# Kernel optimization log

Measured on AMD Instinct MI355X. Metric: run time of the kernel, lower is better.

Reference implementation:

```python
import jax, jax.numpy as jnp
import numpy as np

V, E, H, L, B = 32000, 512, 512, 64, 32
H2 = 2 * H  # decoder hidden size
SOS = 127


def lstm_cell(x, h, c, Wih, Whh, b):
    gates = x @ Wih.T + h @ Whh.T + b
    i, f, g, o = jnp.split(gates, 4, axis=-1)
    i = jax.nn.sigmoid(i); f = jax.nn.sigmoid(f); o = jax.nn.sigmoid(o)
    g = jnp.tanh(g)
    c2 = f * c + i * g
    return o * jnp.tanh(c2), c2


def setup_inputs() -> dict:
    key = jax.random.key(0)
    ks = jax.random.split(key, 20)
    s = 0.02
    inp = {
        "x": jax.random.randint(ks[0], (B, L), 0, V),
        "enc_embed": s * jax.random.normal(ks[1], (V, E), jnp.float32),
        "ef_Wih": s * jax.random.normal(ks[2], (4 * H, E), jnp.float32),
        "ef_Whh": s * jax.random.normal(ks[3], (4 * H, H), jnp.float32),
        "ef_b": jnp.zeros((4 * H,), jnp.float32),
        "eb_Wih": s * jax.random.normal(ks[4], (4 * H, E), jnp.float32),
        "eb_Whh": s * jax.random.normal(ks[5], (4 * H, H), jnp.float32),
        "eb_b": jnp.zeros((4 * H,), jnp.float32),
        "dec_embed": s * jax.random.normal(ks[6], (V, H2), jnp.float32),
        "attn_W": s * jax.random.normal(ks[7], (L, 2 * H2), jnp.float32),
        "attn_b": jnp.zeros((L,), jnp.float32),
        "comb_W": s * jax.random.normal(ks[8], (H2, 2 * H2), jnp.float32),
        "comb_b": jnp.zeros((H2,), jnp.float32),
        "d_Wih": s * jax.random.normal(ks[9], (4 * H2, H2), jnp.float32),
        "d_Whh": s * jax.random.normal(ks[10], (4 * H2, H2), jnp.float32),
        "d_b": jnp.zeros((4 * H2,), jnp.float32),
        "out_W": s * jax.random.normal(ks[11], (V, H2), jnp.float32),
        "out_b": jnp.zeros((V,), jnp.float32),
    }
    return inp


def reference(x, enc_embed, ef_Wih, ef_Whh, ef_b, eb_Wih, eb_Whh, eb_b,
              dec_embed, attn_W, attn_b, comb_W, comb_b,
              d_Wih, d_Whh, d_b, out_W, out_b):
    b, seq = x.shape
    emb = enc_embed[x]  # (B, L, E)

    # Encoder: per-timestep bidirectional LSTM cells (each length-1 call),
    # state carried across the unrolled timestep loop.
    def enc_step(carry, xt):
        hf, cf, hb, cb = carry
        hf, cf = lstm_cell(xt, hf, cf, ef_Wih, ef_Whh, ef_b)
        hb, cb = lstm_cell(xt, hb, cb, eb_Wih, eb_Whh, eb_b)
        return (hf, cf, hb, cb), jnp.concatenate([hf, hb], axis=-1)

    z = jnp.zeros((b, ef_Whh.shape[1]), emb.dtype)
    _, enc_outs = jax.lax.scan(enc_step, (z, z, z, z), emb.transpose(1, 0, 2))
    enc_outs = enc_outs.transpose(1, 0, 2)  # (B, L, 2H)

    # Decoder: Bahdanau-style attention + LSTM cell, greedy argmax feedback.
    h2 = d_Whh.shape[1]

    def dec_step(carry, _):
        h, c, tok = carry
        e = dec_embed[tok]  # (B, 2H)
        aw = jax.nn.softmax(jnp.concatenate([e, h], -1) @ attn_W.T + attn_b, axis=-1)  # (B, L)
        ctx = jnp.einsum('bl,bld->bd', aw, enc_outs)  # (B, 2H)
        comb = jax.nn.relu(jnp.concatenate([e, ctx], -1) @ comb_W.T + comb_b)
        h, c = lstm_cell(comb, h, c, d_Wih, d_Whh, d_b)
        logits = jax.nn.log_softmax(h @ out_W.T + out_b, axis=-1)  # (B, V)
        tok = jnp.argmax(logits, axis=-1)
        return (h, c, tok), logits

    h0 = jnp.zeros((b, h2), emb.dtype)
    tok0 = jnp.full((b,), SOS, dtype=x.dtype)
    _, logits = jax.lax.scan(dec_step, (h0, h0, tok0), None, length=seq)
    return logits.transpose(1, 0, 2)  # (B, T, V)
```

## Files before the change

### kernel.cpp

```cpp
#include <hip/hip_runtime.h>
#include <hip/hip_bf16.h>
#include <string.h>

typedef __bf16 bf16;
typedef __attribute__((ext_vector_type(8))) __bf16 bf16x8;
typedef __attribute__((ext_vector_type(2))) __bf16 bf16x2;
typedef __attribute__((ext_vector_type(4))) float  f32x4;
typedef unsigned long long u64;
typedef unsigned char u8;

#define DEV __device__ __forceinline__

constexpr int V = 32000, E = 512, H = 512, L = 64, NB = 32, H2 = 1024, T = 64, SOS = 127;
constexpr int GE = 4 * H;
constexpr int NBLK = 256;

constexpr size_t OFF_GIN    = 0;
constexpr size_t SZ_GIN     = (size_t)2*T*NB*GE*4;
constexpr size_t OFF_ENCOUT = OFF_GIN + SZ_GIN;
constexpr size_t SZ_ENCOUT  = (size_t)NB*L*H2*2;
constexpr size_t OFF_ENCH   = OFF_ENCOUT + SZ_ENCOUT;
constexpr size_t SZ_ENCH    = (size_t)2*2*NB*H*2;
constexpr size_t OFF_DECH   = OFF_ENCH + SZ_ENCH;
constexpr size_t SZ_DECH    = (size_t)2*NB*H2*2;
constexpr size_t OFF_CAT2   = OFF_DECH + SZ_DECH;
constexpr size_t SZ_CAT2    = (size_t)NB*2*H2*2;
constexpr size_t OFF_COMB   = OFF_CAT2 + SZ_CAT2;
constexpr size_t SZ_COMB    = (size_t)NB*H2*2;
constexpr size_t OFF_HH     = OFF_COMB + SZ_COMB;
constexpr size_t SZ_HH      = (size_t)NB*4*H2*4;
constexpr size_t OFF_PMAX   = OFF_HH + SZ_HH;
constexpr size_t SZ_P       = (size_t)2*NBLK*NB*4;
constexpr size_t OFF_PSUM   = OFF_PMAX + SZ_P;
constexpr size_t OFF_PIDX   = OFF_PSUM + SZ_P;
constexpr size_t OFF_LOGZ   = OFF_PIDX + SZ_P;
constexpr size_t SZ_LOGZ    = (size_t)T*NB*4;
constexpr size_t OFF_WEFIH  = OFF_LOGZ + SZ_LOGZ;
constexpr size_t SZ_WENC    = (size_t)GE*E*2;
constexpr size_t OFF_WEFHH  = OFF_WEFIH + SZ_WENC;
constexpr size_t OFF_WEBIH  = OFF_WEFHH + SZ_WENC;
constexpr size_t OFF_WEBHH  = OFF_WEBIH + SZ_WENC;
constexpr size_t OFF_WCOMB  = OFF_WEBHH + SZ_WENC;
constexpr size_t SZ_WCOMB   = (size_t)H2*2*H2*2;
constexpr size_t OFF_WDIH   = OFF_WCOMB + SZ_WCOMB;
constexpr size_t SZ_WDEC    = (size_t)4*H2*H2*2;
constexpr size_t OFF_WDHH   = OFF_WDIH + SZ_WDEC;
constexpr size_t OFF_WOUT   = OFF_WDHH + SZ_WDEC;
constexpr size_t OFF_WOUT8  = OFF_WOUT;
constexpr size_t SZ_WOUT8   = (size_t)V*1024;
constexpr size_t OFF_WDHH8  = OFF_WOUT8 + SZ_WOUT8;
constexpr size_t SZ_WOUT    = (size_t)V*H2*2;
constexpr size_t OFF_WATTN  = OFF_WOUT + SZ_WOUT;
constexpr size_t SZ_WATTN   = (size_t)L*2*H2*2;
constexpr size_t OFF_EMB2   = OFF_WATTN + SZ_WATTN;
constexpr size_t SZ_EMB2    = (size_t)T*NB*E*2;
constexpr size_t OFF_BAR    = OFF_EMB2 + SZ_EMB2;
constexpr int TAG_PT = 0, TAG_C2 = 8192, TAG_CB = 9216, TAG_H = 11264, TAG_E = 13312;
constexpr int BAR_INTS = 15360;
constexpr size_t OFF_H8 = OFF_BAR + 131072;

constexpr int SM_HL   = 114688;
constexpr int SM_CATF = 114688;
constexpr int SM_REDM = 122880;
constexpr int SM_REDS = 124928;
constexpr int SM_REDI = 126976;
constexpr int SM_SCR  = 129024;
constexpr int SM_BYTES = 147456;

DEV f32x4 mfma16(bf16x8 a, bf16x8 b, f32x4 c) {
  return __builtin_amdgcn_mfma_f32_16x16x32_bf16(a, b, c, 0, 0, 0);
}
DEV f32x4 mfma8(long a, long b, f32x4 c) {
  return __builtin_amdgcn_mfma_f32_16x16x32_fp8_fp8(a, b, c, 0, 0, 0);
}
DEV float sigm(float x) { return 1.f / (1.f + __expf(-x)); }
DEV bf16x8 ld8(const bf16* p) { return *(const bf16x8*)p; }

union U16 { u64 u[2]; bf16x8 v8; f32x4 f4; };
union U4  { unsigned int u; bf16x2 v2; float f; };

DEV bf16x8 ld8_dev(const bf16* p) {
  U16 r;
  r.u[0] = __hip_atomic_load((const u64*)p,       __ATOMIC_RELAXED, __HIP_MEMORY_SCOPE_AGENT);
  r.u[1] = __hip_atomic_load((const u64*)(p + 4), __ATOMIC_RELAXED, __HIP_MEMORY_SCOPE_AGENT);
  return r.v8;
}
DEV void st8_dev(bf16* p, bf16x8 v) {
  U16 r; r.v8 = v;
  __hip_atomic_store((u64*)p,       r.u[0], __ATOMIC_RELAXED, __HIP_MEMORY_SCOPE_AGENT);
  __hip_atomic_store((u64*)(p + 4), r.u[1], __ATOMIC_RELAXED, __HIP_MEMORY_SCOPE_AGENT);
}
DEV void st16f_dev(float* p, f32x4 v) {
  U16 r; r.f4 = v;
  __hip_atomic_store((u64*)p,       r.u[0], __ATOMIC_RELAXED, __HIP_MEMORY_SCOPE_AGENT);
  __hip_atomic_store((u64*)(p + 2), r.u[1], __ATOMIC_RELAXED, __HIP_MEMORY_SCOPE_AGENT);
}
DEV float ldf_dev(const float* p) {
  return __hip_atomic_load(p, __ATOMIC_RELAXED, __HIP_MEMORY_SCOPE_AGENT);
}
DEV void stf_dev(float* p, float v) {
  __hip_atomic_store(p, v, __ATOMIC_RELAXED, __HIP_MEMORY_SCOPE_AGENT);
}
DEV int ldi_dev(const int* p) {
  return __hip_atomic_load(p, __ATOMIC_RELAXED, __HIP_MEMORY_SCOPE_AGENT);
}
DEV void sti_dev(int* p, int v) {
  __hip_atomic_store(p, v, __ATOMIC_RELAXED, __HIP_MEMORY_SCOPE_AGENT);
}
DEV void stb_dev(bf16* p, float x) {
  bf16 h = (bf16)x; unsigned short s; memcpy(&s, &h, 2);
  __hip_atomic_store((unsigned short*)p, s, __ATOMIC_RELAXED, __HIP_MEMORY_SCOPE_AGENT);
}
DEV void st2b_dev(bf16* p, bf16x2 v) {
  U4 r; r.v2 = v;
  __hip_atomic_store((unsigned int*)p, r.u, __ATOMIC_RELAXED, __HIP_MEMORY_SCOPE_AGENT);
}
DEV void stb8_dev(u8* p, u8 v) {
  __hip_atomic_store(p, v, __ATOMIC_RELAXED, __HIP_MEMORY_SCOPE_AGENT);
}
DEV u64 ldu64_dev(const u8* p) {
  return __hip_atomic_load((const u64*)p, __ATOMIC_RELAXED, __HIP_MEMORY_SCOPE_AGENT);
}

DEV void tpub(int* tags, int slot, int ep) {
  __syncthreads();
  if (threadIdx.x == 0)
    sti_dev(tags + slot*32, ep);
}
DEV void twait(int* tags, int n, int ep) {
  if ((int)threadIdx.x < n)
    while (ldi_dev(tags + threadIdx.x*32) < ep)
      __builtin_amdgcn_s_sleep(1);
  asm volatile("" ::: "memory");
  __syncthreads();
}

struct ConvJobs { const float* src[7]; bf16* dst[7]; long n8[7]; };

__global__ __launch_bounds__(256) void k_convert_all(ConvJobs J) {
  long i0 = (long)blockIdx.x * 256 + threadIdx.x;
  long stride = (long)gridDim.x * 256;
  for (int j = 0; j < 7; ++j) {
    const float* __restrict__ src = J.src[j];
    bf16* __restrict__ dst = J.dst[j];
    long n8 = J.n8[j];
    for (long g = i0; g < n8; g += stride) {
      long o = g * 8;
      float4 a = *(const float4*)(src + o);
      float4 b = *(const float4*)(src + o + 4);
      bf16x8 v;
      v[0]=(bf16)a.x; v[1]=(bf16)a.y; v[2]=(bf16)a.z; v[3]=(bf16)a.w;
      v[4]=(bf16)b.x; v[5]=(bf16)b.y; v[6]=(bf16)b.z; v[7]=(bf16)b.w;
      *(bf16x8*)(dst + o) = v;
    }
  }
}

__global__ __launch_bounds__(256) void k_conv_fp8(const float* __restrict__ wsrc,
                                                  const float* __restrict__ hsrc,
                                                  u8* __restrict__ wdst,
                                                  u8* __restrict__ hdst) {
  const long G1 = (long)V*64, G2 = (long)4096*64;
  for (long id = (long)blockIdx.x*256 + threadIdx.x; id < G1 + G2;
       id += (long)gridDim.x*256) {
    const float* s; u8* d; long n, g;
    if (id < G1) { n = id >> 6; g = id & 63; s = wsrc + n*1024 + g*16;
                   d = wdst + n*1024 + ((g ^ (n & 7)) << 4); }
    else { long j = id - G1; n = j >> 6; g = j & 63; s = hsrc + n*1024 + g*16;
           d = hdst + n*1024 + ((g ^ (n & 7)) << 4); }
    unsigned int wv[4];
#pragma unroll
    for (int q = 0; q < 4; ++q) {
      float4 f = *(const float4*)(s + q*4);
      int lo = __builtin_amdgcn_cvt_pk_fp8_f32(f.x*8.f, f.y*8.f, 0, false);
      int hi = __builtin_amdgcn_cvt_pk_fp8_f32(f.z*8.f, f.w*8.f, 0, false);
      wv[q] = (lo & 0xFFFF) | (hi << 16);
    }
    *(uint4*)d = make_uint4(wv[0], wv[1], wv[2], wv[3]);
  }
}

__global__ __launch_bounds__(256) void k_gather_emb(const int* __restrict__ x,
                                                    const float* __restrict__ embed,
                                                    bf16* __restrict__ emb2) {
  int gid = blockIdx.x * 256 + threadIdx.x;
  int m = gid >> 6, k8 = (gid & 63) * 8;
  int b = m & 31, t = m >> 5;
  int tok = x[b * L + t];
  const float* src = embed + (long)tok * E + k8;
  float4 a = *(const float4*)src;
  float4 c = *(const float4*)(src + 4);
  bf16x8 v;
  v[0]=(bf16)a.x; v[1]=(bf16)a.y; v[2]=(bf16)a.z; v[3]=(bf16)a.w;
  v[4]=(bf16)c.x; v[5]=(bf16)c.y; v[6]=(bf16)c.z; v[7]=(bf16)c.w;
  *(bf16x8*)(emb2 + (long)m * E + k8) = v;
}

__global__ __launch_bounds__(256) void k_init(bf16* ench, bf16* dech, float* hh,
                                              int* bar) {
  int i = blockIdx.x * 256 + threadIdx.x;
  hh[i] = 0.f;
  if (i < 2*NB*H)  ench[i] = (bf16)0.f;
  if (i < NB*H2)   dech[i] = (bf16)0.f;
  if (i < BAR_INTS) bar[i] = 0;
}

__global__ __launch_bounds__(256) void k_enc_ingemm(
    const bf16* __restrict__ emb2,
    const bf16* __restrict__ fWih, const float* __restrict__ fB,
    const bf16* __restrict__ bWih, const float* __restrict__ bB,
    float* __restrict__ gin)
{
  int wid  = blockIdx.x * 4 + (threadIdx.x >> 6);
  int lane = threadIdx.x & 63;
  int dir  = wid >> 11;
  int w2   = wid & 2047;
  int m0   = (w2 >> 5) * 32;
  int n0   = (w2 & 31) * 64;
  const bf16*  Wih  = dir ? bWih : fWih;
  const float* Bias = dir ? bB : fB;
  int col = lane & 15, kq = lane >> 4, r4 = kq * 4;

  const bf16* arow[4];
#pragma unroll
  for (int nt = 0; nt < 4; ++nt) arow[nt] = Wih + (long)(n0 + nt*16 + col)*E + kq*8;
  const bf16* brow[2];
#pragma unroll
  for (int mt = 0; mt < 2; ++mt) brow[mt] = emb2 + (long)(m0 + mt*16 + col)*E + kq*8;

  f32x4 acc[2][4] = {};
  for (int kk = 0; kk < E/32; ++kk) {
    bf16x8 a[4], bv[2];
#pragma unroll
    for (int nt = 0; nt < 4; ++nt) a[nt] = ld8(arow[nt] + kk*32);
#pragma unroll
    for (int mt = 0; mt < 2; ++mt) bv[mt] = ld8(brow[mt] + kk*32);
#pragma unroll
    for (int mt = 0; mt < 2; ++mt)
#pragma unroll
      for (int nt = 0; nt < 4; ++nt)
        acc[mt][nt] = mfma16(a[nt], bv[mt], acc[mt][nt]);
  }
#pragma unroll
  for (int mt = 0; mt < 2; ++mt) {
    int m = m0 + mt*16 + col;
    int b = m & 31, t = m >> 5;
    float* gp = gin + ((long)(dir*T + t)*NB + b)*GE;
#pragma unroll
    for (int nt = 0; nt < 4; ++nt) {
      int nb = n0 + nt*16 + r4;
      f32x4 v = acc[mt][nt];
      float4 o;
      o.x = v[0] + Bias[nb+0];
      o.y = v[1] + Bias[nb+1];
      o.z = v[2] + Bias[nb+2];
      o.w = v[3] + Bias[nb+3];
      *(float4*)(gp + nb) = o;
    }
  }
}

struct EncArgs {
  const bf16* fWhh; const bf16* bWhh; const float* gin;
  bf16* ench; bf16* encout; int* etag;
};

__global__ __launch_bounds__(256, 1) void k_encoder(EncArgs A) {
  __shared__ float lds[4][16][32];
  int tid = threadIdx.x, w = tid >> 6, lane = tid & 63;
  int dir = blockIdx.x >> 5, j0 = (blockIdx.x & 31) * 16;
  int col = lane & 15, kq = lane >> 4, r4 = kq*4;
  const bf16* Whh = dir ? A.bWhh : A.fWhh;
  const bf16* arow = Whh + (long)(w*H + j0 + col)*H + kq*8;
  int* myTags = A.etag + dir*32*32;
  float creg0 = 0.f, creg1 = 0.f;

  for (int t = 0; t < T; ++t) {
    if (t > 0) twait(myTags, 32, t);
    const bf16* hbase = A.ench + (t&1)*(2*NB*H) + dir*(NB*H);
    bf16*       hout  = A.ench + ((t&1)^1)*(2*NB*H) + dir*(NB*H);
    const bf16* b0 = hbase + col*H + kq*8;
    const bf16* b1 = hbase + (16+col)*H + kq*8;
    f32x4 a0 = {}, a1 = {};
    for (int kk = 0; kk < H/32; ++kk) {
      bf16x8 a = ld8(arow + kk*32);
      a0 = mfma16(a, ld8_dev(b0 + kk*32), a0);
      a1 = mfma16(a, ld8_dev(b1 + kk*32), a1);
    }
#pragma unroll
    for (int r = 0; r < 4; ++r) { lds[w][r4+r][col] = a0[r]; lds[w][r4+r][16+col] = a1[r]; }
    __syncthreads();
    const float* gp = A.gin + (long)(dir*T + t)*NB*GE;
    {
      int jj = tid >> 5, b = tid & 31, j = j0 + jj;
      const float* g4 = gp + (long)b*GE;
      float i_ = sigm(lds[0][jj][b] + g4[0*H + j]);
      float f_ = sigm(lds[1][jj][b] + g4[1*H + j]);
      float g_ = tanhf(lds[2][jj][b] + g4[2*H + j]);
      float o_ = sigm(lds[3][jj][b] + g4[3*H + j]);
      float c2 = f_*creg0 + i_*g_; creg0 = c2;
      float hv = o_*tanhf(c2);
      stb_dev(hout + b*H + j, hv);
      A.encout[((long)b*L + t)*H2 + dir*H + j] = (bf16)hv;
    }
    {
      int idx = tid + 256, jj = idx >> 5, b = idx & 31, j = j0 + jj;
      const float* g4 = gp + (long)b*GE;
      float i_ = sigm(lds[0][jj][b] + g4[0*H + j]);
      float f_ = sigm(lds[1][jj][b] + g4[1*H + j]);
      float g_ = tanhf(lds[2][jj][b] + g4[2*H + j]);
      float o_ = sigm(lds[3][jj][b] + g4[3*H + j]);
      float c2 = f_*creg1 + i_*g_; creg1 = c2;
      float hv = o_*tanhf(c2);
      stb_dev(hout + b*H + j, hv);
      A.encout[((long)b*L + t)*H2 + dir*H + j] = (bf16)hv;
    }
    tpub(myTags, blockIdx.x & 31, t + 1);
  }
}

struct DecArgs {
  const float* dec_embed; const bf16* wattn; const float* attn_b;
  const bf16* encout;
  const bf16* wcomb; const float* comb_b;
  const bf16* wdih; const float* db;
  const u8* wout8; const u8* wdhh8; const float* outb;
  bf16* dech; u8* hout8; float* hh; bf16* cat2; bf16* comb;
  float* pmax; float* psum; int* pidx; float* logz; float* out;
  int* tags;
};

__global__ __launch_bounds__(512, 1) void k_decoder(DecArgs A) {
  __shared__ __attribute__((aligned(16))) char smem[SM_BYTES];
  __shared__ float aw[64];
  __shared__ int   stok;
  float* catF = (float*)(smem + SM_CATF);
  float* redm = (float*)(smem + SM_REDM);
  float* reds = (float*)(smem + SM_REDS);
  int*   redi = (int*)  (smem + SM_REDI);
  float* scr  = (float*)(smem + SM_SCR);

  int* PT  = A.tags + TAG_PT;
  int* C2T = A.tags + TAG_C2;
  int* CBT = A.tags + TAG_CB;
  int* HT  = A.tags + TAG_H;

  int tid = threadIdx.x, bid = blockIdx.x;
  int w = tid >> 6, lane = tid & 63;
  int col = lane & 15, kq = lane >> 4, r4 = kq*4;
  float creg = 0.f;

  int ntot = (bid < 48) ? 8 : 9;
  int tstart = (bid < 48) ? bid*8 : 384 + 9*(bid - 48);
  const int nlds = 7;

  for (int i = 0; i < nlds; ++i) {
    int tn = tstart + i;
    const u8* src = (tn < 2000) ? A.wout8 + (long)tn*16384
                                : A.wdhh8 + (long)(tn - 2000)*16384;
#pragma unroll
    for (int rr = 0; rr < 2; ++rr) {
      int flat = rr*8192 + w*1024 + lane*16;
      __builtin_amdgcn_global_load_lds(
          (const __attribute__((address_space(1))) void*)(src + flat),
          (__attribute__((address_space(3))) void*)(smem + i*16384 + rr*8192 + w*1024),
          16, 0, 0);
    }
  }
  asm volatile("s_waitcnt vmcnt(0)" ::: "memory");
  __syncthreads();

  for (int t = 0; t < T; ++t) {
    const bf16* hin  = A.dech + (t&1)*(NB*H2);
    bf16*       hout = A.dech + ((t&1)^1)*(NB*H2);
    float* pmaxP = A.pmax + ((t&1)^1)*NBLK*32;
    float* psumP = A.psum + ((t&1)^1)*NBLK*32;
    int*   pidxP = A.pidx + ((t&1)^1)*NBLK*32;

    if (bid < NB) {
      int b = bid;
      if (t > 0) {
        twait(PT, NBLK, t);
        float m = -1e30f, s = 0.f; int id = 0;
        if (tid < 256) {
          m  = ldf_dev(pmaxP + tid*32 + b);
          s  = ldf_dev(psumP + tid*32 + b);
          id = ldi_dev(pidxP + tid*32 + b);
#pragma unroll
          for (int off = 1; off < 64; off <<= 1) {
            float om = __shfl_xor(m, off);
            float os = __shfl_xor(s, off);
            int   oi = __shfl_xor(id, off);
            s += os;
            if (om > m || (om == m && oi < id)) { m = om; id = oi; }
          }
          if (lane == 0) { redm[w] = m; reds[w] = s; redi[w] = id; }
        }
        __syncthreads();
        if (tid == 0) {
          float mm = redm[0]; int ii2 = redi[0];
          float ss = reds[0] + reds[1] + reds[2] + reds[3];
#pragma unroll
          for (int q = 1; q < 4; ++q) {
            if (redm[q] > mm || (redm[q] == mm && redi[q] < ii2)) { mm = redm[q]; ii2 = redi[q]; }
          }
          A.logz[(t-1)*32 + b] = logf(ss);
          stok = ii2;
        }
      } else if (tid == 0) stok = SOS;
      __syncthreads();
      int tok = stok;

      const float* erow = A.dec_embed + (long)tok*H2;
      bf16* c2row = A.cat2 + (long)b*(2*H2);
      if (tid < 128) {
        int o = tid*8;
        float4 a = *(const float4*)(erow + o);
        float4 c = *(const float4*)(erow + o + 4);
        catF[o+0]=a.x; catF[o+1]=a.y; catF[o+2]=a.z; catF[o+3]=a.w;
        catF[o+4]=c.x; catF[o+5]=c.y; catF[o+6]=c.z; catF[o+7]=c.w;
        bf16x8 v;
        v[0]=(bf16)a.x; v[1]=(bf16)a.y; v[2]=(bf16)a.z; v[3]=(bf16)a.w;
        v[4]=(bf16)c.x; v[5]=(bf16)c.y; v[6]=(bf16)c.z; v[7]=(bf16)c.w;
        st8_dev(c2row + o, v);
      } else if (tid < 256) {
        int o = (tid - 128)*8;
        bf16x8 hv = ld8_dev(hin + (long)b*H2 + o);
#pragma unroll
        for (int e = 0; e < 8; ++e) catF[H2 + o + e] = (float)hv[e];
      }
      __syncthreads();

      {
        int l = tid >> 3, q = tid & 7;
        const bf16*  wrow = A.wattn + (long)l*(2*H2) + q*256;
        const float* crow = catF + q*256;
        float sacc = 0.f;
        for (int k = 0; k < 256; k += 8) {
          bf16x8 wv = ld8(wrow + k);
#pragma unroll
          for (int e = 0; e < 8; ++e) sacc += (float)wv[e] * crow[k+e];
        }
        sacc += __shfl_xor(sacc, 1);
        sacc += __shfl_xor(sacc, 2);
        sacc += __shfl_xor(sacc, 4);
        if (q == 0) aw[l] = sacc + A.attn_b[l];
      }
      __syncthreads();

      if (tid < 64) {
        float v = aw[tid];
        float m = v;
#pragma unroll
        for (int off = 1; off < 64; off <<= 1) m = fmaxf(m, __shfl_xor(m, off));
        float p = __expf(v - m);
        float s = p;
#pragma unroll
        for (int off = 1; off < 64; off <<= 1) s += __shfl_xor(s, off);
        aw[tid] = p / s;
      }
      __syncthreads();

      {
        int grp = tid >> 7, jt = tid & 127;
        int j8 = jt * 8;
        const bf16* eo = A.encout + (long)b*L*H2 + j8;
        float acc[8] = {};
        for (int l = grp*16; l < grp*16 + 16; ++l) {
          float a = aw[l];
          bf16x8 v = ld8(eo + (long)l*H2);
#pragma unroll
          for (int e = 0; e < 8; ++e) acc[e] += a*(float)v[e];
        }
#pragma unroll
        for (int e = 0; e < 8; ++e) scr[grp*1024 + j8 + e] = acc[e];
      }
      __syncthreads();
      {
        int j2 = tid * 2;
        bf16x2 o;
#pragma unroll
        for (int e = 0; e < 2; ++e) {
          int j = j2 + e;
          o[e] = (bf16)(scr[j] + scr[1024+j] + scr[2048+j] + scr[3072+j]);
        }
        st2b_dev(c2row + H2 + j2, o);
      }
      tpub(C2T, bid, t + 1);
    }

    if (bid < 64) {
      twait(C2T, 32, t + 1);
      int n0 = bid * 16;
      const bf16* arow = A.wcomb + (long)(n0 + col)*(2*H2) + w*256 + kq*8;
      const bf16* b0 = A.cat2 + (long)col*(2*H2) + w*256 + kq*8;
      const bf16* b1 = A.cat2 + (long)(16+col)*(2*H2) + w*256 + kq*8;
      f32x4 a0 = {}, a1 = {};
      for (int kk = 0; kk < 8; ++kk) {
        bf16x8 a = ld8(arow + kk*32);
        a0 = mfma16(a, ld8_dev(b0 + kk*32), a0);
        a1 = mfma16(a, ld8_dev(b1 + kk*32), a1);
      }
#pragma unroll
      for (int r = 0; r < 4; ++r) {
        scr[(w*2+0)*256 + (r4+r)*16 + col] = a0[r];
        scr[(w*2+1)*256 + (r4+r)*16 + col] = a1[r];
      }
      __syncthreads();
      {
        int r = tid >> 5, b = tid & 31;
        int bt = b >> 4, cb = b & 15;
        float v = 0.f;
#pragma unroll
        for (int g = 0; g < 8; ++g) v += scr[(g*2+bt)*256 + r*16 + cb];
        v += A.comb_b[n0 + r];
        stb_dev(A.comb + (long)b*H2 + n0 + r, fmaxf(v, 0.f));
      }
      tpub(CBT, bid, t + 1);
    }

    if (bid < 64) {
      twait(CBT, 64, t + 1);
      int j0 = bid * 16;
      int g = w >> 1, half = w & 1;
      const bf16* arow = A.wdih + (long)(g*H2 + j0 + col)*H2 + half*512 + kq*8;
      const bf16* b0 = A.comb + (long)col*H2 + half*512 + kq*8;
      const bf16* b1 = A.comb + (long)(16+col)*H2 + half*512 + kq*8;
      f32x4 a0 = {}, a1 = {};
      for (int kk = 0; kk < 16; ++kk) {
        bf16x8 a = ld8(arow + kk*32);
        a0 = mfma16(a, ld8_dev(b0 + kk*32), a0);
        a1 = mfma16(a, ld8_dev(b1 + kk*32), a1);
      }
#pragma unroll
      for (int r = 0; r < 4; ++r) {
        scr[(w*2+0)*256 + (r4+r)*16 + col] = a0[r];
        scr[(w*2+1)*256 + (r4+r)*16 + col] = a1[r];
      }
      __syncthreads();
      {
        int jj = tid >> 5, b = tid & 31, j = j0 + jj;
        int bt = b >> 4, cb = b & 15;
#define GV(gg) (scr[((2*(gg)+0)*2+bt)*256 + jj*16 + cb] + scr[((2*(gg)+1)*2+bt)*256 + jj*16 + cb] \
                + A.db[(gg)*H2 + j] + ldf_dev(A.hh + (long)b*(4*H2) + (gg)*H2 + j))
        float i_ = sigm(GV(0));
        float f_ = sigm(GV(1));
        float g_ = tanhf(GV(2));
        float o_ = sigm(GV(3));
#undef GV
        float c2 = f_*creg + i_*g_; creg = c2;
        float hv = o_*tanhf(c2);
        stb_dev(hout + b*H2 + j, hv);
        int q8 = __builtin_amdgcn_cvt_pk_fp8_f32(hv*16.f, hv*16.f, 0, false);
        stb8_dev(A.hout8 + b*1024 + j, (u8)(q8 & 0xFF));
      }
      tpub(HT, bid, t + 1);
    }

    {
      twait(HT, 64, t + 1);
      float* pmaxW = A.pmax + (t&1)*NBLK*32;
      float* psumW = A.psum + (t&1)*NBLK*32;
      int*   pidxW = A.pidx + (t&1)*NBLK*32;

#pragma unroll
      for (int k2 = 0; k2 < 4; ++k2) {
        int id = k2*512 + tid;
        int r = id >> 6, g = id & 63;
        const u8* sp = A.hout8 + r*1024 + g*16;
        u64 lo = ldu64_dev(sp);
        u64 hi = ldu64_dev(sp + 8);
        char* dp = smem + SM_HL + r*1024 + ((g ^ (r & 7)) << 4);
        *(u64*)dp = lo; *(u64*)(dp + 8) = hi;
      }
      __syncthreads();

      float pm[2] = {-1e30f, -1e30f};
      float ps[2] = {0.f, 0.f};
      int  pid[2] = {0, 0};

      for (int ii = 0; ii < 2; ++ii) {
        if (ii == 1 && (w != 0 || ntot < 9)) break;
        int ti = (ii == 0) ? w : 8;
        int tn = tstart + ti;
        f32x4 acc0 = {}, acc1 = {};
        if (ti < nlds) {
          const char* Ab = smem + ti*16384 + col*1024;
          const char* Hb = smem + SM_HL + col*1024;
#pragma unroll 8
          for (int ks = 0; ks < 32; ++ks) {
            int off = (((ks*2 + (kq>>1)) ^ (col & 7)) << 4) + (kq & 1)*8;
            long a  = *(const long*)(Ab + off);
            long b0 = *(const long*)(Hb + off);
            long b1 = *(const long*)(Hb + 16*1024 + off);
            acc0 = mfma8(a, b0, acc0);
            acc1 = mfma8(a, b1, acc1);
          }
        } else {
          const u8* Ab = ((tn < 2000) ? A.wout8 + (long)tn*16384
                                      : A.wdhh8 + (long)(tn - 2000)*16384) + col*1024;
          const char* Hb = smem + SM_HL + col*1024;
#pragma unroll 8
          for (int ks = 0; ks < 32; ++ks) {
            int off = (((ks*2 + (kq>>1)) ^ (col & 7)) << 4) + (kq & 1)*8;
            long a  = (long)ldu64_dev(Ab + off);
            long b0 = *(const long*)(Hb + off);
            long b1 = *(const long*)(Hb + 16*1024 + off);
            acc0 = mfma8(a, b0, acc0);
            acc1 = mfma8(a, b1, acc1);
          }
        }
        if (tn < 2000) {
          int nb = tn*16 + kq*4;
#pragma unroll
          for (int bt = 0; bt < 2; ++bt) {
            int b = col + bt*16;
            f32x4 v = bt ? acc1 : acc0;
            f32x4 o;
#pragma unroll
            for (int r = 0; r < 4; ++r) {
              float xv = v[r]*0.0078125f + A.outb[nb + r];
              o[r] = xv;
              ps[bt] += __expf(xv);
              if (xv > pm[bt]) { pm[bt] = xv; pid[bt] = nb + r; }
            }
            __builtin_nontemporal_store(o, (f32x4*)(A.out + ((long)b*T + t)*V + nb));
          }
        } else {
          int nb = (tn - 2000)*16 + kq*4;
#pragma unroll
          for (int bt = 0; bt < 2; ++bt) {
            int b = col + bt*16;
            f32x4 v = bt ? acc1 : acc0;
#pragma unroll
            for (int r = 0; r < 4; ++r) v[r] *= 0.0078125f;
            st16f_dev(A.hh + (long)b*(4*H2) + nb, v);
          }
        }
      }
#pragma unroll
      for (int off = 16; off <= 32; off <<= 1) {
#pragma unroll
        for (int bt = 0; bt < 2; ++bt) {
          float om = __shfl_xor(pm[bt], off);
          float os = __shfl_xor(ps[bt], off);
          int   oi = __shfl_xor(pid[bt], off);
          ps[bt] += os;
          if (om > pm[bt] || (om == pm[bt] && oi < pid[bt])) { pm[bt] = om; pid[bt] = oi; }
        }
      }
      __syncthreads();
      float* dm = (float*)(smem + SM_HL);
      float* ds = dm + 256;
      int*   di = (int*)(ds + 256);
      if (lane < 16) {
#pragma unroll
        for (int bt = 0; bt < 2; ++bt) {
          int b = bt*16 + lane;
          dm[w*32 + b] = pm[bt];
          ds[w*32 + b] = ps[bt];
          di[w*32 + b] = pid[bt];
        }
      }
      __syncthreads();
      if (tid < 32) {
        int b = tid;
        float m = -1e30f, s = 0.f; int id = 0;
#pragma unroll
        for (int r = 0; r < 8; ++r) {
          float om = dm[r*32 + b]; int oi = di[r*32 + b];
          s += ds[r*32 + b];
          if (om > m || (om == m && oi < id)) { m = om; id = oi; }
        }
        stf_dev(pmaxW + bid*32 + b, m);
        stf_dev(psumW + bid*32 + b, s);
        sti_dev(pidxW + bid*32 + b, id);
      }
      tpub(PT, bid, t + 1);
    }
  }

  if (bid < NB) {
    twait(PT, NBLK, T);
    int b = bid;
    const float* psumP = A.psum + ((T-1)&1)*NBLK*32;
    float s = 0.f;
    if (tid < 256) {
      s = ldf_dev(psumP + tid*32 + b);
#pragma unroll
      for (int off = 1; off < 64; off <<= 1) s += __shfl_xor(s, off);
      if (lane == 0) reds[w] = s;
    }
    __syncthreads();
    if (tid == 0) A.logz[(T-1)*32 + b] = logf(reds[0] + reds[1] + reds[2] + reds[3]);
  }
}

__global__ __launch_bounds__(256) void k_fixup(float* __restrict__ out,
                                               const float* __restrict__ logz)
{
  long i = (long)blockIdx.x * 256 + threadIdx.x;
  long stride = (long)gridDim.x * 256;
  long total = (long)NB * T * V / 4;
  for (long g = i; g < total; g += stride) {
    long flat = g * 4;
    long bt = flat / V;
    int tt = (int)(bt & 63), b = (int)(bt >> 6);
    float lz = logz[tt*32 + b];
    f32x4 v = *(const f32x4*)(out + flat);
    v[0] -= lz; v[1] -= lz; v[2] -= lz; v[3] -= lz;
    __builtin_nontemporal_store(v, (f32x4*)(out + flat));
  }
}

extern "C" void kernel_launch(void* const* d_in, const int* in_sizes, int n_in,
                              void* d_out, int out_size, void* d_ws, size_t ws_size,
                              hipStream_t stream)
{
  const int*   x         = (const int*)  d_in[0];
  const float* enc_embed = (const float*)d_in[1];
  const float* ef_Wih    = (const float*)d_in[2];
  const float* ef_Whh    = (const float*)d_in[3];
  const float* ef_b      = (const float*)d_in[4];
  const float* eb_Wih    = (const float*)d_in[5];
  const float* eb_Whh    = (const float*)d_in[6];
  const float* eb_b      = (const float*)d_in[7];
  const float* dec_embed = (const float*)d_in[8];
  const float* attn_W    = (const float*)d_in[9];
  const float* attn_b    = (const float*)d_in[10];
  const float* comb_W    = (const float*)d_in[11];
  const float* comb_b    = (const float*)d_in[12];
  const float* d_Wih     = (const float*)d_in[13];
  const float* d_Whh     = (const float*)d_in[14];
  const float* d_b       = (const float*)d_in[15];
  const float* out_W     = (const float*)d_in[16];
  const float* out_b     = (const float*)d_in[17];
  float* out = (float*)d_out;
  char* ws = (char*)d_ws;

  float* gin    = (float*)(ws + OFF_GIN);
  bf16*  encout = (bf16*) (ws + OFF_ENCOUT);
  bf16*  ench   = (bf16*) (ws + OFF_ENCH);
  bf16*  dech   = (bf16*) (ws + OFF_DECH);
  bf16*  cat2   = (bf16*) (ws + OFF_CAT2);
  bf16*  comb   = (bf16*) (ws + OFF_COMB);
  float* hh     = (float*)(ws + OFF_HH);
  float* pmax   = (float*)(ws + OFF_PMAX);
  float* psum   = (float*)(ws + OFF_PSUM);
  int*   pidx   = (int*)  (ws + OFF_PIDX);
  float* logz   = (float*)(ws + OFF_LOGZ);
  bf16*  wefih  = (bf16*) (ws + OFF_WEFIH);
  bf16*  wefhh  = (bf16*) (ws + OFF_WEFHH);
  bf16*  webih  = (bf16*) (ws + OFF_WEBIH);
  bf16*  webhh  = (bf16*) (ws + OFF_WEBHH);
  bf16*  wcomb  = (bf16*) (ws + OFF_WCOMB);
  bf16*  wdih   = (bf16*) (ws + OFF_WDIH);
  u8*    wout8  = (u8*)   (ws + OFF_WOUT8);
  u8*    wdhh8  = (u8*)   (ws + OFF_WDHH8);
  bf16*  wattn  = (bf16*) (ws + OFF_WATTN);
  bf16*  emb2   = (bf16*) (ws + OFF_EMB2);
  int*   bar    = (int*)  (ws + OFF_BAR);
  u8*    hout8  = (u8*)   (ws + OFF_H8);

  ConvJobs J;
  J.src[0]=ef_Wih; J.dst[0]=wefih; J.n8[0]=(long)GE*E/8;
  J.src[1]=ef_Whh; J.dst[1]=wefhh; J.n8[1]=(long)GE*H/8;
  J.src[2]=eb_Wih; J.dst[2]=webih; J.n8[2]=(long)GE*E/8;
  J.src[3]=eb_Whh; J.dst[3]=webhh; J.n8[3]=(long)GE*H/8;
  J.src[4]=comb_W; J.dst[4]=wcomb; J.n8[4]=(long)H2*2*H2/8;
  J.src[5]=d_Wih;  J.dst[5]=wdih;  J.n8[5]=(long)4*H2*H2/8;
  J.src[6]=attn_W; J.dst[6]=wattn; J.n8[6]=(long)L*2*H2/8;
  hipLaunchKernelGGL(k_convert_all, dim3(2048), dim3(256), 0, stream, J);
  hipLaunchKernelGGL(k_conv_fp8, dim3(2048), dim3(256), 0, stream,
                     out_W, d_Whh, wout8, wdhh8);
  hipLaunchKernelGGL(k_gather_emb, dim3(512), dim3(256), 0, stream, x, enc_embed, emb2);
  hipLaunchKernelGGL(k_init, dim3(512), dim3(256), 0, stream, ench, dech, hh, bar);
  hipLaunchKernelGGL(k_enc_ingemm, dim3(1024), dim3(256), 0, stream,
                     emb2, wefih, ef_b, webih, eb_b, gin);

  EncArgs EA = { wefhh, webhh, gin, ench, encout, bar + TAG_E };
  hipLaunchKernelGGL(k_encoder, dim3(64), dim3(256), 0, stream, EA);

  DecArgs DA = { dec_embed, wattn, attn_b, encout, wcomb, comb_b,
                 wdih, d_b, wout8, wdhh8, out_b,
                 dech, hout8, hh, cat2, comb, pmax, psum, pidx, logz, out,
                 bar };
  hipLaunchKernelGGL(k_decoder, dim3(256), dim3(512), 0, stream, DA);

  hipLaunchKernelGGL(k_fixup, dim3(2048), dim3(256), 0, stream, out, logz);
}
```

Before: 4.812 ms.

## Keep spilled fp8 weight tiles in registers and split comb wait per wave

The fp8 weight tiles that do not fit in LDS are now loaded into 32 per-lane registers once before the time loop, instead of being re-read from global memory every decoder step. A new per-block tag is published after the embedding half of the concat buffer is written, so comb waves that consume only that half (w<4) wait on it while the other waves still wait for the context half. This shortens the critical path of each serial step. In exchange it costs 64 extra VGPRs per thread, which may cause spills under the 512-thread launch bound, and adds another tag array.

```diff
diff --git a/kernel.cpp b/kernel.cpp
--- a/kernel.cpp
+++ b/kernel.cpp
@@ -56,7 +56,8 @@
 constexpr size_t SZ_EMB2    = (size_t)T*NB*E*2;
 constexpr size_t OFF_BAR    = OFF_EMB2 + SZ_EMB2;
 constexpr int TAG_PT = 0, TAG_C2 = 8192, TAG_CB = 9216, TAG_H = 11264, TAG_E = 13312;
-constexpr int BAR_INTS = 15360;
+constexpr int TAG_TE = 15360;
+constexpr int BAR_INTS = 16384;
 constexpr size_t OFF_H8 = OFF_BAR + 131072;
 
 constexpr int SM_HL   = 114688;
@@ -133,6 +134,14 @@
       __builtin_amdgcn_s_sleep(1);
   asm volatile("" ::: "memory");
   __syncthreads();
+}
+DEV void twait_wave(int* tags, int n, int ep) {
+  int l = threadIdx.x & 63;
+  if (l < n)
+    while (ldi_dev(tags + l*32) < ep)
+      __builtin_amdgcn_s_sleep(1);
+  __builtin_amdgcn_wave_barrier();
+  asm volatile("" ::: "memory");
 }
 
 struct ConvJobs { const float* src[7]; bf16* dst[7]; long n8[7]; };
@@ -344,6 +353,7 @@
   int* C2T = A.tags + TAG_C2;
   int* CBT = A.tags + TAG_CB;
   int* HT  = A.tags + TAG_H;
+  int* TET = A.tags + TAG_TE;
 
   int tid = threadIdx.x, bid = blockIdx.x;
   int w = tid >> 6, lane = tid & 63;
@@ -365,6 +375,24 @@
           (const __attribute__((address_space(1))) void*)(src + flat),
           (__attribute__((address_space(3))) void*)(smem + i*16384 + rr*8192 + w*1024),
           16, 0, 0);
+    }
+  }
+  u64 sreg[32];
+  {
+    int myTile = -1;
+    if (w == 7 && ntot >= 8) myTile = tstart + 7;
+    if (w == 0 && ntot == 9) myTile = tstart + 8;
+    if (myTile >= 0) {
+      const u8* Ab = ((myTile < 2000) ? A.wout8 + (long)myTile*16384
+                                      : A.wdhh8 + (long)(myTile - 2000)*16384) + col*1024;
+#pragma unroll
+      for (int ks = 0; ks < 32; ++ks) {
+        int off = (((ks*2 + (kq>>1)) ^ (col & 7)) << 4) + (kq & 1)*8;
+        sreg[ks] = *(const u64*)(Ab + off);
+      }
+    } else {
+#pragma unroll
+      for (int ks = 0; ks < 32; ++ks) sreg[ks] = 0;
     }
   }
   asm volatile("s_waitcnt vmcnt(0)" ::: "memory");
@@ -429,7 +457,7 @@
 #pragma unroll
         for (int e = 0; e < 8; ++e) catF[H2 + o + e] = (float)hv[e];
       }
-      __syncthreads();
+      tpub(TET, bid, t + 1);
 
       {
         int l = tid >> 3, q = tid & 7;
@@ -490,7 +518,8 @@
     }
 
     if (bid < 64) {
-      twait(C2T, 32, t + 1);
+      if (w < 4) twait_wave(TET, 32, t + 1);
+      else       twait_wave(C2T, 32, t + 1);
       int n0 = bid * 16;
       const bf16* arow = A.wcomb + (long)(n0 + col)*(2*H2) + w*256 + kq*8;
       const bf16* b0 = A.cat2 + (long)col*(2*H2) + w*256 + kq*8;
@@ -584,9 +613,9 @@
         int ti = (ii == 0) ? w : 8;
         int tn = tstart + ti;
         f32x4 acc0 = {}, acc1 = {};
+        const char* Hb = smem + SM_HL + col*1024;
         if (ti < nlds) {
           const char* Ab = smem + ti*16384 + col*1024;
-          const char* Hb = smem + SM_HL + col*1024;
 #pragma unroll 8
           for (int ks = 0; ks < 32; ++ks) {
             int off = (((ks*2 + (kq>>1)) ^ (col & 7)) << 4) + (kq & 1)*8;
@@ -597,13 +626,10 @@
             acc1 = mfma8(a, b1, acc1);
           }
         } else {
-          const u8* Ab = ((tn < 2000) ? A.wout8 + (long)tn*16384
-                                      : A.wdhh8 + (long)(tn - 2000)*16384) + col*1024;
-          const char* Hb = smem + SM_HL + col*1024;
-#pragma unroll 8
+#pragma unroll
           for (int ks = 0; ks < 32; ++ks) {
             int off = (((ks*2 + (kq>>1)) ^ (col & 7)) << 4) + (kq & 1)*8;
-            long a  = (long)ldu64_dev(Ab + off);
+            long a  = (long)sreg[ks];
             long b0 = *(const long*)(Hb + off);
             long b1 = *(const long*)(Hb + 16*1024 + off);
             acc0 = mfma8(a, b0, acc0);
```

Measured after the change: 5.353 ms. 1.11x slower.
